# Kernel tuning notes

Measured on AMD Instinct MI355X. Metric: run time of the kernel, lower is better.

The kernel has to match this reference:

```python
import jax, jax.numpy as jnp
import numpy as np

NUM_HEADS = 16
WINDOW = 256


def setup_inputs() -> dict:
    key = jax.random.key(0)
    ks = jax.random.split(key, 9)
    B, S, H = 2, 2048, 1024
    sc = 0.02
    return {
        "hidden_states": jax.random.normal(ks[0], (B, S, H), jnp.float32),
        "wq": jax.random.normal(ks[1], (H, H), jnp.float32) * sc,
        "bq": jax.random.normal(ks[2], (H,), jnp.float32) * sc,
        "wk": jax.random.normal(ks[3], (H, H), jnp.float32) * sc,
        "bk": jax.random.normal(ks[4], (H,), jnp.float32) * sc,
        "wv": jax.random.normal(ks[5], (H, H), jnp.float32) * sc,
        "bv": jax.random.normal(ks[6], (H,), jnp.float32) * sc,
        "wo": jax.random.normal(ks[7], (H, H), jnp.float32) * sc,
        "bo": jax.random.normal(ks[8], (H,), jnp.float32) * sc,
    }


def reference(hidden_states, wq, bq, wk, bk, wv, bv, wo, bo):
    B, S, H = hidden_states.shape
    nH, hd = NUM_HEADS, H // NUM_HEADS
    scale = 1.0 / np.sqrt(hd).astype(np.float32)

    def heads(x):  # [B,S,H] -> [B,nH,S,hd]
        return x.reshape(B, S, nH, hd).transpose(0, 2, 1, 3)

    q = heads(hidden_states @ wq.T + bq)
    k = heads(hidden_states @ wk.T + bk)
    v = heads(hidden_states @ wv.T + bv)

    scores = jnp.einsum("bhqd,bhkd->bhqk", q, k) * scale  # [B,nH,S,S]

    # allowed keys for query i: j in [i - WINDOW, i] (causal window)
    i = jnp.arange(S)[:, None]
    j = jnp.arange(S)[None, :]
    allowed = (j <= i) & (j >= i - WINDOW)  # [S,S]

    scores = jnp.where(allowed[None, None], scores, -jnp.inf)
    # original clamps AFTER masking -> -inf becomes -10000 (soft mask)
    scores = jnp.clip(scores, -10000.0, 10000.0)

    probs = jax.nn.softmax(scores, axis=-1)
    probs = jnp.nan_to_num(probs, nan=0.0, posinf=0.0, neginf=0.0)

    out = jnp.einsum("bhqk,bhkd->bhqd", probs, v)  # [B,nH,S,hd]
    out = out.transpose(0, 2, 1, 3).reshape(B, S, H)
    return out @ wo.T + bo
```

## Files before the change

### kernel.cpp

```cpp
#include <hip/hip_runtime.h>
#include <hip/hip_bf16.h>
#include <stdint.h>

typedef __attribute__((ext_vector_type(8))) short short8;
typedef __attribute__((ext_vector_type(4))) float f32x4;
typedef __attribute__((ext_vector_type(4))) unsigned short u16x4;

__device__ __forceinline__ float bf2f(unsigned short u) {
  union { unsigned int u; float f; } x; x.u = ((unsigned int)u) << 16; return x.f;
}
__device__ __forceinline__ unsigned short f2bf(float f) {
  union { float f; unsigned int u; } x; x.f = f;
  unsigned int u = x.u;
  return (unsigned short)((u + 0x7fffu + ((u >> 16) & 1u)) >> 16);
}

__device__ __forceinline__ void gload_lds16(const void* g, void* l) {
  __builtin_amdgcn_global_load_lds(
      (const __attribute__((address_space(1))) void*)g,
      (__attribute__((address_space(3))) void*)l, 16, 0, 0);
}

__global__ void cvt_all(const float* __restrict__ X,
                        const float* __restrict__ w0, const float* __restrict__ w1,
                        const float* __restrict__ w2, const float* __restrict__ w3,
                        unsigned short* __restrict__ Xb,
                        unsigned short* __restrict__ Wb,
                        unsigned short* __restrict__ Ones) {
  if (blockIdx.y == 0) {
    int i = (blockIdx.x * 256 + threadIdx.x) * 4;
    f32x4 f = *(const f32x4*)(X + i);
    u16x4 o = { f2bf(f[0]), f2bf(f[1]), f2bf(f[2]), f2bf(f[3]) };
    *(u16x4*)(Xb + i) = o;
  } else if (blockIdx.y == 1) {
    int wi = blockIdx.x >> 10;
    const float* s = wi == 0 ? w0 : wi == 1 ? w1 : wi == 2 ? w2 : w3;
    int j = ((blockIdx.x & 1023) * 256 + threadIdx.x) * 4;
    f32x4 f = *(const f32x4*)(s + j);
    u16x4 o = { f2bf(f[0]), f2bf(f[1]), f2bf(f[2]), f2bf(f[3]) };
    *(u16x4*)(Wb + ((size_t)wi << 20) + j) = o;
  } else {
    if (blockIdx.x < 32) {
      int j = (blockIdx.x * 256 + threadIdx.x) * 4;
      unsigned short v = (j < 2048) ? (unsigned short)0x3F80 : (unsigned short)0;
      u16x4 o = { v, v, v, v };
      *(u16x4*)(Ones + j) = o;
    }
  }
}

__global__ __launch_bounds__(512, 2)
void gemm_qkv_fused(const unsigned short* __restrict__ A,
                    const unsigned short* __restrict__ Wbase,
                    const float* __restrict__ bq, const float* __restrict__ bk,
                    const float* __restrict__ bv,
                    unsigned short* __restrict__ obf) {
  const int K = 1024, NT = 32;
  constexpr int ASZ = 128 * 32;
  constexpr int BSZ = 3 * 128 * 32;
  __shared__ unsigned short lds[3 * (ASZ + BSZ)];

  int flat = blockIdx.y * 8 + blockIdx.x;
  int swz = (flat & 7) * 32 + (flat >> 3);
  const int n0 = (swz & 7) * 128, m0 = (swz >> 3) * 128;

  const int tid = threadIdx.x, lane = tid & 63, w = tid >> 6;
  const int wr = w >> 1, wc = w & 1;
  const int fr = lane & 15, g = lane >> 4;

  f32x4 acc[3][2][4] = {};

#define STAGE_A(bi, t)                                                          \
  do {                                                                          \
    int s = tid;                                                                \
    int row = s >> 2;                                                           \
    int gc = (s & 3) ^ ((row >> 1) & 3);                                        \
    gload_lds16(A + (size_t)(m0 + row) * K + (t) * 32 + gc * 8,                 \
                &lds[(bi) * (ASZ + BSZ) + s * 8]);                              \
  } while (0)

#define STAGE_W(bi, t, i)                                                       \
  do {                                                                          \
    int s = (i) * 512 + tid;                                                    \
    int row = s >> 2;                                                           \
    int zz = row >> 7, br = row & 127;                                          \
    int gc = (s & 3) ^ ((row >> 1) & 3);                                        \
    gload_lds16(Wbase + ((size_t)zz << 20) + (size_t)(n0 + br) * K +            \
                    (t) * 32 + gc * 8,                                          \
                &lds[(bi) * (ASZ + BSZ) + ASZ + s * 8]);                        \
  } while (0)

  STAGE_A(0, 0); STAGE_W(0, 0, 0); STAGE_W(0, 0, 1); STAGE_W(0, 0, 2);
  STAGE_A(1, 1); STAGE_W(1, 1, 0); STAGE_W(1, 1, 1); STAGE_W(1, 1, 2);

  for (int t = 0; t < NT; ++t) {
    if (t < NT - 1)
      asm volatile("s_waitcnt vmcnt(4)" ::: "memory");
    else
      asm volatile("s_waitcnt vmcnt(0)" ::: "memory");
    __builtin_amdgcn_s_barrier();
    __builtin_amdgcn_sched_barrier(0);

    const int bi = t % 3, bi2 = (t + 2) % 3;
    const bool pf = (t + 2 < NT);
    unsigned short* lb = lds + bi * (ASZ + BSZ);

    if (pf) STAGE_A(bi2, t + 2);

    short8 af[2];
#pragma unroll
    for (int m = 0; m < 2; ++m) {
      int ra = wr * 32 + m * 16 + fr;
      af[m] = *(const short8*)&lb[ra * 32 + ((g ^ ((ra >> 1) & 3)) * 8)];
    }

#pragma unroll
    for (int zz = 0; zz < 3; ++zz) {
      short8 bfr[4];
#pragma unroll
      for (int n = 0; n < 4; ++n) {
        int rb2 = zz * 128 + wc * 64 + n * 16 + fr;
        bfr[n] = *(const short8*)&lb[ASZ + rb2 * 32 + ((g ^ ((rb2 >> 1) & 3)) * 8)];
      }
      if (pf) STAGE_W(bi2, t + 2, zz);
      __builtin_amdgcn_s_setprio(1);
#pragma unroll
      for (int m = 0; m < 2; ++m)
#pragma unroll
        for (int n = 0; n < 4; ++n) {
          if (zz < 2)
            acc[zz][m][n] = __builtin_amdgcn_mfma_f32_16x16x32_bf16(
                bfr[n], af[m], acc[zz][m][n], 0, 0, 0);
          else
            acc[zz][m][n] = __builtin_amdgcn_mfma_f32_16x16x32_bf16(
                af[m], bfr[n], acc[zz][m][n], 0, 0, 0);
        }
      __builtin_amdgcn_s_setprio(0);
    }
  }
#undef STAGE_A
#undef STAGE_W

#pragma unroll
  for (int zz = 0; zz < 2; ++zz) {
    const float* bias = zz == 0 ? bq : bk;
#pragma unroll
    for (int m = 0; m < 2; ++m) {
#pragma unroll
      for (int n = 0; n < 4; ++n) {
        int token = m0 + wr * 32 + m * 16 + fr;
        int col0 = n0 + wc * 64 + n * 16 + g * 4;
        f32x4 bvv = *(const f32x4*)&bias[col0];
        u16x4 pk;
#pragma unroll
        for (int i = 0; i < 4; ++i) pk[i] = f2bf(acc[zz][m][n][i] + bvv[i]);
        int hh = col0 >> 6, d0 = col0 & 63;
        int bb = token >> 11, s0 = token & 2047;
        *(u16x4*)&obf[(((size_t)(zz * 32 + bb * 16 + hh)) * 2048 + s0) * 64 + d0] = pk;
      }
    }
  }
#pragma unroll
  for (int m = 0; m < 2; ++m) {
#pragma unroll
    for (int n = 0; n < 4; ++n) {
      int col = n0 + wc * 64 + n * 16 + fr;
      float bias_v = bv[col];
      int row0 = m0 + wr * 32 + m * 16 + g * 4;
      int hh = col >> 6, d = col & 63;
      int bb = row0 >> 11, s0 = row0 & 2047;
      u16x4 pk;
#pragma unroll
      for (int i = 0; i < 4; ++i) pk[i] = f2bf(acc[2][m][n][i] + bias_v);
      *(u16x4*)&obf[(((size_t)(64 + bb * 16 + hh)) * 64 + d) * 2048 + s0] = pk;
    }
  }
}

__global__ __launch_bounds__(512, 2)
void gemm_oproj(const unsigned short* __restrict__ A,
                const unsigned short* __restrict__ W,
                const float* __restrict__ bias, float* __restrict__ of32) {
  const int K = 1024, NT = 16;
  constexpr int ABUF = 128 * 64;
  constexpr int BUFSZ = 2 * ABUF;
  __shared__ unsigned short lds[3 * BUFSZ];

  int flat = blockIdx.y * 8 + blockIdx.x;
  int swz = (flat & 7) * 32 + (flat >> 3);
  const int n0 = (swz & 7) * 128, m0 = (swz >> 3) * 128;

  const int tid = threadIdx.x, lane = tid & 63, w = tid >> 6;
  const int kg = w >> 2, wq = w & 3;
  const int mt = (wq >> 1) * 64, nt = (wq & 1) * 64;
  const int fr = lane & 15, g = lane >> 4;

  f32x4 acc[4][4] = {};

#define STAGE(bi, t)                                                            \
  do {                                                                          \
    unsigned short* lb = lds + (bi) * BUFSZ;                                    \
    _Pragma("unroll") for (int i = 0; i < 2; ++i) {                             \
      int c = i * 512 + tid;                                                    \
      int row = c >> 3;                                                         \
      int ch = (c & 7) ^ (row & 7);                                             \
      gload_lds16(A + (size_t)(m0 + row) * K + (t) * 64 + ch * 8, &lb[c * 8]);  \
    }                                                                           \
    _Pragma("unroll") for (int i = 0; i < 2; ++i) {                             \
      int c = i * 512 + tid;                                                    \
      int row = c >> 3;                                                         \
      int ch = (c & 7) ^ (row & 7);                                             \
      gload_lds16(W + (size_t)(n0 + row) * K + (t) * 64 + ch * 8,               \
                  &lb[ABUF + c * 8]);                                           \
    }                                                                           \
  } while (0)

  STAGE(0, 0);
  STAGE(1, 1);
  const int kc = kg * 4 + g;
  for (int t = 0; t < NT; ++t) {
    if (t < NT - 1)
      asm volatile("s_waitcnt vmcnt(4)" ::: "memory");
    else
      asm volatile("s_waitcnt vmcnt(0)" ::: "memory");
    __builtin_amdgcn_s_barrier();
    __builtin_amdgcn_sched_barrier(0);
    if (t + 2 < NT) STAGE((t + 2) % 3, t + 2);

    unsigned short* lb = lds + (t % 3) * BUFSZ;
    short8 af[4], bf[4];
#pragma unroll
    for (int m = 0; m < 4; ++m) {
      int ra = mt + m * 16 + fr;
      af[m] = *(const short8*)&lb[ra * 64 + ((kc ^ (ra & 7)) * 8)];
    }
#pragma unroll
    for (int n = 0; n < 4; ++n) {
      int rb = nt + n * 16 + fr;
      bf[n] = *(const short8*)&lb[ABUF + rb * 64 + ((kc ^ (rb & 7)) * 8)];
    }
    __builtin_amdgcn_s_setprio(1);
#pragma unroll
    for (int m = 0; m < 4; ++m)
#pragma unroll
      for (int n = 0; n < 4; ++n)
        acc[m][n] = __builtin_amdgcn_mfma_f32_16x16x32_bf16(bf[n], af[m],
                                                            acc[m][n], 0, 0, 0);
    __builtin_amdgcn_s_setprio(0);
  }
#undef STAGE

  __syncthreads();
  float* red = (float*)lds;
  if (kg == 1) {
#pragma unroll
    for (int m = 0; m < 4; ++m)
#pragma unroll
      for (int n = 0; n < 4; ++n)
        *(f32x4*)(red + wq * 4096 + (m * 4 + n) * 256 + lane * 4) = acc[m][n];
  }
  __syncthreads();
  if (kg == 0) {
#pragma unroll
    for (int m = 0; m < 4; ++m) {
#pragma unroll
      for (int n = 0; n < 4; ++n) {
        f32x4 other = *(const f32x4*)(red + wq * 4096 + (m * 4 + n) * 256 + lane * 4);
        int token = m0 + mt + m * 16 + fr;
        int col0 = n0 + nt + n * 16 + g * 4;
        f32x4 bvv = *(const f32x4*)&bias[col0];
        f32x4 o;
#pragma unroll
        for (int i = 0; i < 4; ++i) o[i] = acc[m][n][i] + other[i] + bvv[i];
        *(f32x4*)&of32[(size_t)token * 1024 + col0] = o;
      }
    }
  }
}

__global__ __launch_bounds__(256)
void attn_mfma(const unsigned short* __restrict__ QKV,
               const unsigned short* __restrict__ Ones,
               unsigned short* __restrict__ AO) {
  const int S = 2048;
  const int b = blockIdx.z, h = blockIdx.y;
  const int q0 = blockIdx.x * 128;
  const size_t hb = (size_t)(b * 16 + h);
  const unsigned short* Qh = QKV + hb * (S * 64);
  const unsigned short* Kh = QKV + 4194304 + hb * (S * 64);
  const unsigned short* Vt = QKV + 8388608 + hb * (S * 64);

  const int tid = threadIdx.x;
  const int lane = tid & 63, w = tid >> 6;
  const int c = lane & 15, g = lane >> 4;
  const int qw0 = q0 + 32 * w;

  __shared__ unsigned short Plds[4][1024];
  char* Pb = (char*)&Plds[w][0];

  short8 qa[2][2];
#pragma unroll
  for (int mi = 0; mi < 2; ++mi)
#pragma unroll
    for (int cs = 0; cs < 2; ++cs)
      qa[mi][cs] = *(const short8*)(Qh + (size_t)(qw0 + 16 * mi + c) * 64 + 32 * cs + g * 8);

  f32x4 o[2][5] = {};

  int kt0 = qw0 - 256; if (kt0 < 0) kt0 = 0;
  const int ktlast = qw0;

  short8 kf[2][2], vf[5];
#pragma unroll
  for (int ni = 0; ni < 2; ++ni)
#pragma unroll
    for (int cs = 0; cs < 2; ++cs)
      kf[ni][cs] = *(const short8*)(Kh + (size_t)(kt0 + 16 * ni + c) * 64 + 32 * cs + g * 8);
#pragma unroll
  for (int ni = 0; ni < 4; ++ni)
    vf[ni] = *(const short8*)(Vt + (size_t)(16 * ni + c) * 2048 + kt0 + g * 8);
  vf[4] = *(const short8*)(Ones + (size_t)c * 2048 + kt0 + g * 8);

  for (int kt = kt0; kt <= ktlast; kt += 32) {
    const int ktn = (kt + 32 <= ktlast) ? kt + 32 : kt;
    short8 kfn[2][2], vfn[5];
#pragma unroll
    for (int ni = 0; ni < 2; ++ni)
#pragma unroll
      for (int cs = 0; cs < 2; ++cs)
        kfn[ni][cs] = *(const short8*)(Kh + (size_t)(ktn + 16 * ni + c) * 64 + 32 * cs + g * 8);
#pragma unroll
    for (int ni = 0; ni < 4; ++ni)
      vfn[ni] = *(const short8*)(Vt + (size_t)(16 * ni + c) * 2048 + ktn + g * 8);
    vfn[4] = *(const short8*)(Ones + (size_t)c * 2048 + ktn + g * 8);

    f32x4 sA[2][2] = {};
#pragma unroll
    for (int mi = 0; mi < 2; ++mi)
#pragma unroll
      for (int ni = 0; ni < 2; ++ni)
#pragma unroll
        for (int cs = 0; cs < 2; ++cs)
          sA[mi][ni] = __builtin_amdgcn_mfma_f32_16x16x32_bf16(qa[mi][cs], kf[ni][cs],
                                                               sA[mi][ni], 0, 0, 0);

#pragma unroll
    for (int mi = 0; mi < 2; ++mi) {
#pragma unroll
      for (int ni = 0; ni < 2; ++ni) {
#pragma unroll
        for (int r = 0; r < 4; ++r) {
          int q = qw0 + 16 * mi + 4 * g + r;
          int k = kt + 16 * ni + c;
          float p = ((unsigned)(q - k) <= 256u) ? __expf(sA[mi][ni][r] * 0.125f) : 0.f;
          int qloc = 16 * mi + 4 * g + r;
          int xr = (qloc & 12) << 2;
          *(unsigned short*)(Pb + ((qloc * 64 + ni * 32 + c * 2) ^ xr)) = f2bf(p);
        }
      }
    }

#pragma unroll
    for (int mi = 0; mi < 2; ++mi) {
      int qloc = 16 * mi + c;
      short8 pa = *(const short8*)(Pb + ((qloc * 64 + g * 16) ^ ((qloc & 12) << 2)));
#pragma unroll
      for (int ni = 0; ni < 5; ++ni)
        o[mi][ni] = __builtin_amdgcn_mfma_f32_16x16x32_bf16(pa, vf[ni], o[mi][ni], 0, 0, 0);
    }

#pragma unroll
    for (int ni = 0; ni < 2; ++ni)
#pragma unroll
      for (int cs = 0; cs < 2; ++cs)
        kf[ni][cs] = kfn[ni][cs];
#pragma unroll
    for (int ni = 0; ni < 5; ++ni)
      vf[ni] = vfn[ni];
  }

#pragma unroll
  for (int mi = 0; mi < 2; ++mi)
#pragma unroll
    for (int r = 0; r < 4; ++r) {
      float ls = __shfl(o[mi][4][r], lane & 48);
      float inv = 1.f / ls;
      int q = qw0 + 16 * mi + 4 * g + r;
      unsigned short* row = AO + (size_t)(b * 2048 + q) * 1024 + h * 64 + c;
#pragma unroll
      for (int ni = 0; ni < 4; ++ni)
        row[16 * ni] = f2bf(o[mi][ni][r] * inv);
    }
}

extern "C" void kernel_launch(void* const* d_in, const int* in_sizes, int n_in,
                              void* d_out, int out_size, void* d_ws, size_t ws_size,
                              hipStream_t stream) {
  const float* X  = (const float*)d_in[0];
  const float* wq = (const float*)d_in[1];
  const float* bq = (const float*)d_in[2];
  const float* wk = (const float*)d_in[3];
  const float* bk = (const float*)d_in[4];
  const float* wv = (const float*)d_in[5];
  const float* bv = (const float*)d_in[6];
  const float* wo = (const float*)d_in[7];
  const float* bo = (const float*)d_in[8];
  float* out = (float*)d_out;

  unsigned short* Xb   = (unsigned short*)d_ws;
  unsigned short* Wb   = Xb + 4194304;
  unsigned short* QKV  = Wb + 4194304;
  unsigned short* AO   = QKV + 12582912;
  unsigned short* Ones = AO + 4194304;

  cvt_all<<<dim3(4096, 3), dim3(256), 0, stream>>>(X, wq, wk, wv, wo, Xb, Wb, Ones);
  gemm_qkv_fused<<<dim3(8, 32), dim3(512), 0, stream>>>(Xb, Wb, bq, bk, bv, QKV);
  attn_mfma<<<dim3(16, 16, 2), dim3(256), 0, stream>>>(QKV, Ones, AO);
  gemm_oproj<<<dim3(8, 32), dim3(512), 0, stream>>>(AO, Wb + 3 * 1048576, bo, out);
}
```

Before: 84.36 us.

## Retile output projection GEMM to 128x64 tiles without split-K reduction

The output projection GEMM moves from 128x128 tiles with 512 threads and an intra-block split-K (two k-groups reduced through LDS) to 128x64 tiles with 256 threads and no split-K. Each wave now covers 64x32 outputs and loops over both k-halves itself. The grid doubles to 512 blocks, which fills more CUs on the device and drops the LDS reduction and its extra barriers. In exchange each block reuses the A tile less and the kernel issues more global loads for A in total.

```diff
diff --git a/kernel.cpp b/kernel.cpp
--- a/kernel.cpp
+++ b/kernel.cpp
@@ -177,37 +177,37 @@
   }
 }
 
-__global__ __launch_bounds__(512, 2)
+__global__ __launch_bounds__(256)
 void gemm_oproj(const unsigned short* __restrict__ A,
                 const unsigned short* __restrict__ W,
                 const float* __restrict__ bias, float* __restrict__ of32) {
   const int K = 1024, NT = 16;
   constexpr int ABUF = 128 * 64;
-  constexpr int BUFSZ = 2 * ABUF;
+  constexpr int BBUF = 64 * 64;
+  constexpr int BUFSZ = ABUF + BBUF;
   __shared__ unsigned short lds[3 * BUFSZ];
 
-  int flat = blockIdx.y * 8 + blockIdx.x;
-  int swz = (flat & 7) * 32 + (flat >> 3);
-  const int n0 = (swz & 7) * 128, m0 = (swz >> 3) * 128;
+  int flat = blockIdx.y * 16 + blockIdx.x;
+  int swz = (flat & 7) * 64 + (flat >> 3);
+  const int n0 = (swz & 15) * 64, m0 = (swz >> 4) * 128;
 
   const int tid = threadIdx.x, lane = tid & 63, w = tid >> 6;
-  const int kg = w >> 2, wq = w & 3;
-  const int mt = (wq >> 1) * 64, nt = (wq & 1) * 64;
+  const int wr = w >> 1, wc = w & 1;
   const int fr = lane & 15, g = lane >> 4;
 
-  f32x4 acc[4][4] = {};
+  f32x4 acc[4][2] = {};
 
 #define STAGE(bi, t)                                                            \
   do {                                                                          \
     unsigned short* lb = lds + (bi) * BUFSZ;                                    \
-    _Pragma("unroll") for (int i = 0; i < 2; ++i) {                             \
-      int c = i * 512 + tid;                                                    \
+    _Pragma("unroll") for (int i = 0; i < 4; ++i) {                             \
+      int c = i * 256 + tid;                                                    \
       int row = c >> 3;                                                         \
       int ch = (c & 7) ^ (row & 7);                                             \
       gload_lds16(A + (size_t)(m0 + row) * K + (t) * 64 + ch * 8, &lb[c * 8]);  \
     }                                                                           \
     _Pragma("unroll") for (int i = 0; i < 2; ++i) {                             \
-      int c = i * 512 + tid;                                                    \
+      int c = i * 256 + tid;                                                    \
       int row = c >> 3;                                                         \
       int ch = (c & 7) ^ (row & 7);                                             \
       gload_lds16(W + (size_t)(n0 + row) * K + (t) * 64 + ch * 8,               \
@@ -217,10 +217,9 @@
 
   STAGE(0, 0);
   STAGE(1, 1);
-  const int kc = kg * 4 + g;
   for (int t = 0; t < NT; ++t) {
     if (t < NT - 1)
-      asm volatile("s_waitcnt vmcnt(4)" ::: "memory");
+      asm volatile("s_waitcnt vmcnt(6)" ::: "memory");
     else
       asm volatile("s_waitcnt vmcnt(0)" ::: "memory");
     __builtin_amdgcn_s_barrier();
@@ -228,52 +227,43 @@
     if (t + 2 < NT) STAGE((t + 2) % 3, t + 2);
 
     unsigned short* lb = lds + (t % 3) * BUFSZ;
-    short8 af[4], bf[4];
-#pragma unroll
-    for (int m = 0; m < 4; ++m) {
-      int ra = mt + m * 16 + fr;
-      af[m] = *(const short8*)&lb[ra * 64 + ((kc ^ (ra & 7)) * 8)];
-    }
-#pragma unroll
-    for (int n = 0; n < 4; ++n) {
-      int rb = nt + n * 16 + fr;
-      bf[n] = *(const short8*)&lb[ABUF + rb * 64 + ((kc ^ (rb & 7)) * 8)];
-    }
-    __builtin_amdgcn_s_setprio(1);
-#pragma unroll
-    for (int m = 0; m < 4; ++m)
-#pragma unroll
-      for (int n = 0; n < 4; ++n)
-        acc[m][n] = __builtin_amdgcn_mfma_f32_16x16x32_bf16(bf[n], af[m],
-                                                            acc[m][n], 0, 0, 0);
-    __builtin_amdgcn_s_setprio(0);
+#pragma unroll
+    for (int kk = 0; kk < 2; ++kk) {
+      const int kc = kk * 4 + g;
+      short8 af[4], bf[2];
+#pragma unroll
+      for (int m = 0; m < 4; ++m) {
+        int ra = wr * 64 + m * 16 + fr;
+        af[m] = *(const short8*)&lb[ra * 64 + ((kc ^ (ra & 7)) * 8)];
+      }
+#pragma unroll
+      for (int n = 0; n < 2; ++n) {
+        int rb = wc * 32 + n * 16 + fr;
+        bf[n] = *(const short8*)&lb[ABUF + rb * 64 + ((kc ^ (rb & 7)) * 8)];
+      }
+      __builtin_amdgcn_s_setprio(1);
+#pragma unroll
+      for (int m = 0; m < 4; ++m)
+#pragma unroll
+        for (int n = 0; n < 2; ++n)
+          acc[m][n] = __builtin_amdgcn_mfma_f32_16x16x32_bf16(bf[n], af[m],
+                                                              acc[m][n], 0, 0, 0);
+      __builtin_amdgcn_s_setprio(0);
+    }
   }
 #undef STAGE
 
-  __syncthreads();
-  float* red = (float*)lds;
-  if (kg == 1) {
-#pragma unroll
-    for (int m = 0; m < 4; ++m)
-#pragma unroll
-      for (int n = 0; n < 4; ++n)
-        *(f32x4*)(red + wq * 4096 + (m * 4 + n) * 256 + lane * 4) = acc[m][n];
-  }
-  __syncthreads();
-  if (kg == 0) {
-#pragma unroll
-    for (int m = 0; m < 4; ++m) {
-#pragma unroll
-      for (int n = 0; n < 4; ++n) {
-        f32x4 other = *(const f32x4*)(red + wq * 4096 + (m * 4 + n) * 256 + lane * 4);
-        int token = m0 + mt + m * 16 + fr;
-        int col0 = n0 + nt + n * 16 + g * 4;
-        f32x4 bvv = *(const f32x4*)&bias[col0];
-        f32x4 o;
-#pragma unroll
-        for (int i = 0; i < 4; ++i) o[i] = acc[m][n][i] + other[i] + bvv[i];
-        *(f32x4*)&of32[(size_t)token * 1024 + col0] = o;
-      }
+#pragma unroll
+  for (int m = 0; m < 4; ++m) {
+#pragma unroll
+    for (int n = 0; n < 2; ++n) {
+      int token = m0 + wr * 64 + m * 16 + fr;
+      int col0 = n0 + wc * 32 + n * 16 + g * 4;
+      f32x4 bvv = *(const f32x4*)&bias[col0];
+      f32x4 o;
+#pragma unroll
+      for (int i = 0; i < 4; ++i) o[i] = acc[m][n][i] + bvv[i];
+      *(f32x4*)&of32[(size_t)token * 1024 + col0] = o;
     }
   }
 }
@@ -416,5 +406,5 @@
   cvt_all<<<dim3(4096, 3), dim3(256), 0, stream>>>(X, wq, wk, wv, wo, Xb, Wb, Ones);
   gemm_qkv_fused<<<dim3(8, 32), dim3(512), 0, stream>>>(Xb, Wb, bq, bk, bv, QKV);
   attn_mfma<<<dim3(16, 16, 2), dim3(256), 0, stream>>>(QKV, Ones, AO);
-  gemm_oproj<<<dim3(8, 32), dim3(512), 0, stream>>>(AO, Wb + 3 * 1048576, bo, out);
-}
+  gemm_oproj<<<dim3(16, 32), dim3(256), 0, stream>>>(AO, Wb + 3 * 1048576, bo, out);
+}
```

Result: no change. 84.81 us (+0.5%).
